# Optimization experiments

Hardware: AMD Instinct MI355X
Metric: run time of the kernel (lower is better)

The kernel has to match this reference:

```python
import jax, jax.numpy as jnp
from jax import lax
import numpy as np

D = 1024      # d_model
H = 16        # n_heads == n_v_heads
DK = 64       # head_k_dim = d_model // n_heads
DV = 128      # head_v_dim = head_dim * expand_v (2.0)
KDIM = H * DK   # 1024
VDIM = H * DV   # 2048
CONV_K = 4
B, T = 2, 4096
EPS = 1e-5


def setup_inputs() -> dict:
    key = jax.random.key(0)
    ks = jax.random.split(key, 14)
    def w(k, shape, s=0.02):
        return jax.random.normal(k, shape, jnp.float32) * s
    return {
        "x": jax.random.normal(ks[0], (B, T, D), jnp.float32),
        "w_q": w(ks[1], (D, KDIM)),
        "w_k": w(ks[2], (D, KDIM)),
        "w_v": w(ks[3], (D, VDIM)),
        "w_a": w(ks[4], (D, H)),
        "w_b": w(ks[5], (D, H)),
        "w_g": w(ks[6], (D, VDIM)),
        "w_out": w(ks[7], (VDIM, D)),
        "A_log": jnp.log(jax.random.uniform(ks[8], (H,), jnp.float32, 1.0, 16.0)),
        "dt_bias": jax.random.uniform(ks[9], (H,), jnp.float32, -4.0, -1.0),
        "conv_q": w(ks[10], (KDIM, CONV_K), 0.1),
        "conv_k": w(ks[11], (KDIM, CONV_K), 0.1),
        "conv_v": w(ks[12], (VDIM, CONV_K), 0.1),
        "norm_w": jnp.ones((DV,), jnp.float32),
    }


def _causal_conv_silu(x, w):
    # x: [B,T,C], w: [C,Kw]  depthwise causal conv1d followed by SiLU
    C = x.shape[-1]
    Kw = w.shape[-1]
    xp = jnp.pad(x, ((0, 0), (Kw - 1, 0), (0, 0))).transpose(0, 2, 1)  # [B,C,T+Kw-1]
    y = lax.conv_general_dilated(
        xp, w[:, None, :], window_strides=(1,), padding="VALID",
        feature_group_count=C, dimension_numbers=("NCH", "OIH", "NCH"))
    return jax.nn.silu(y.transpose(0, 2, 1))  # [B,T,C]


def _l2norm(x, eps=1e-6):
    return x * lax.rsqrt(jnp.sum(x * x, axis=-1, keepdims=True) + eps)


def _gated_delta_rule(q, k, v, g, beta):
    # q,k: [B,T,H,DK] (l2-normalized), v: [B,T,H,DV], g,beta: [B,T,H]
    scale = q.shape[-1] ** -0.5
    qs = jnp.moveaxis(q, 1, 0)
    ks_ = jnp.moveaxis(k, 1, 0)
    vs = jnp.moveaxis(v, 1, 0)
    gs = jnp.moveaxis(g, 1, 0)
    bs = jnp.moveaxis(beta, 1, 0)

    def step(S, inp):
        q_t, k_t, v_t, g_t, b_t = inp
        S = S * jnp.exp(g_t)[..., None, None]            # gated decay
        mem = jnp.einsum("bhk,bhkv->bhv", k_t, S)        # current memory readout
        delta = (v_t - mem) * b_t[..., None]             # beta-weighted delta
        S = S + jnp.einsum("bhk,bhv->bhkv", k_t, delta)  # delta-rule update
        o_t = jnp.einsum("bhk,bhkv->bhv", q_t * scale, S)
        return S, o_t

    S0 = jnp.zeros((q.shape[0], q.shape[2], q.shape[3], v.shape[3]), q.dtype)
    _, o = lax.scan(step, S0, (qs, ks_, vs, gs, bs))
    return jnp.moveaxis(o, 0, 1)  # [B,T,H,DV]


def reference(x, w_q, w_k, w_v, w_a, w_b, w_g, w_out, A_log, dt_bias,
              conv_q, conv_k, conv_v, norm_w):
    Bx, Tx, _ = x.shape
    q = x @ w_q
    k = x @ w_k
    v = x @ w_v
    beta = jax.nn.sigmoid(x @ w_b) * 2.0                      # allow_neg_eigval
    g = -jnp.exp(A_log) * jax.nn.softplus((x @ w_a) + dt_bias)  # [B,T,H]

    q = _causal_conv_silu(q, conv_q)
    k = _causal_conv_silu(k, conv_k)
    v = _causal_conv_silu(v, conv_v)

    q = q.reshape(Bx, Tx, H, DK)
    k = k.reshape(Bx, Tx, H, DK)
    v = v.reshape(Bx, Tx, H, DV)

    # use_qk_l2norm_in_kernel=True
    q = _l2norm(q)
    k = _l2norm(k)

    o = _gated_delta_rule(q, k, v, g, beta)  # [B,T,H,DV]

    # gated RMSNorm: normalize o, gate with silu(w_g(x))
    g_gate = (x @ w_g).reshape(Bx, Tx, H, DV)
    rms = o * lax.rsqrt(jnp.mean(o * o, axis=-1, keepdims=True) + EPS)
    y = rms * norm_w * jax.nn.silu(g_gate)
    return y.reshape(Bx, Tx, VDIM) @ w_out
```

## Files before the change

### kernel.cpp

```cpp
#include <hip/hip_runtime.h>
#include <hip/hip_bf16.h>
#include <math.h>

#define Bc 2
#define Tc 4096
#define Dc 1024
#define Hc 16
#define DKc 64
#define DVc 128
#define KDIMc 1024
#define VDIMc 2048
#define Mrows (Bc*Tc)
#define CC 64
#define NCH (Tc/CC)

typedef short short8 __attribute__((ext_vector_type(8)));
typedef float f32x4 __attribute__((ext_vector_type(4)));

__device__ __forceinline__ float siluf(float x) {
    return x / (1.f + expf(-x));
}
__device__ __forceinline__ float dot4(float4 a, float4 b) {
    return a.x * b.x + a.y * b.y + a.z * b.z + a.w * b.w;
}
__device__ __forceinline__ unsigned short f2bf(float f) {
    unsigned int u = __float_as_uint(f);
    unsigned int r = (u + 0x7fffu + ((u >> 16) & 1u)) >> 16;
    return (unsigned short)r;
}
__device__ __forceinline__ unsigned int pk2(float a, float b) {
    return (unsigned)f2bf(a) | ((unsigned)f2bf(b) << 16);
}
__device__ __forceinline__ float bf2f(unsigned short s) {
    unsigned int u = ((unsigned int)s) << 16;
    return __uint_as_float(u);
}
__device__ __forceinline__ void gload16(const unsigned short* g,
                                        unsigned short* l) {
    __builtin_amdgcn_global_load_lds(
        (const __attribute__((address_space(1))) unsigned int*)g,
        (__attribute__((address_space(3))) unsigned int*)l, 16, 0, 0);
}

__global__ void __launch_bounds__(256) convert_bf16(
    const float* __restrict__ in, unsigned short* __restrict__ out, int n4) {
    int g = blockIdx.x * 256 + threadIdx.x;
    if (g >= n4) return;
    float4 v = *(const float4*)&in[(size_t)g * 4];
    *(uint2*)&out[(size_t)g * 4] = make_uint2(pk2(v.x, v.y), pk2(v.z, v.w));
}

__global__ void __launch_bounds__(256) transp_bf16(
    const float* __restrict__ in, unsigned short* __restrict__ out, int K,
    int N) {
    __shared__ float t[32][33];
    const int nbx = N >> 5;
    const int n0 = (blockIdx.x % nbx) << 5;
    const int k0 = (blockIdx.x / nbx) << 5;
    const int c = threadIdx.x & 31, r4 = (threadIdx.x >> 5) << 2;
#pragma unroll
    for (int i = 0; i < 4; i++)
        t[r4 + i][c] = in[(size_t)(k0 + r4 + i) * N + n0 + c];
    __syncthreads();
#pragma unroll
    for (int i = 0; i < 4; i++)
        out[(size_t)(n0 + r4 + i) * K + k0 + c] = f2bf(t[c][r4 + i]);
}

__global__ void __launch_bounds__(256) transp_f32w(
    const float* __restrict__ in, float* __restrict__ out) {
    __shared__ float t[64][17];
    const int k0 = blockIdx.x * 64;
    const int r = threadIdx.x >> 2, c4 = (threadIdx.x & 3) << 2;
    float4 v = *(const float4*)&in[(size_t)(k0 + r) * 16 + c4];
    t[r][c4 + 0] = v.x;
    t[r][c4 + 1] = v.y;
    t[r][c4 + 2] = v.z;
    t[r][c4 + 3] = v.w;
    __syncthreads();
    const int n = threadIdx.x >> 4;
    const int kk = (threadIdx.x & 15) << 2;
    out[(size_t)n * Dc + k0 + kk + 0] = t[kk + 0][n];
    out[(size_t)n * Dc + k0 + kk + 1] = t[kk + 1][n];
    out[(size_t)n * Dc + k0 + kk + 2] = t[kk + 2][n];
    out[(size_t)n * Dc + k0 + kk + 3] = t[kk + 3][n];
}

__global__ void __launch_bounds__(256) transp_k16(
    const unsigned short* __restrict__ in, unsigned short* __restrict__ out) {
    __shared__ unsigned short t[64][68];
    const int bx = blockIdx.x & 63;
    const int by = (blockIdx.x >> 6) & 15;
    const int b = blockIdx.x >> 10;
    const int t0 = bx << 6, c0 = by << 6;
    {
        const int row = threadIdx.x >> 2, c16 = (threadIdx.x & 3) << 4;
        const unsigned short* src =
            &in[((size_t)b * Tc + t0 + row) * KDIMc + c0 + c16];
#pragma unroll
        for (int i = 0; i < 4; i++)
            *(uint2*)&t[row][c16 + i * 4] = *(const uint2*)&src[i * 4];
    }
    __syncthreads();
    {
        const int cc = threadIdx.x & 63, tp = (threadIdx.x >> 6) << 4;
        unsigned short v[16];
#pragma unroll
        for (int i = 0; i < 16; i++) v[i] = t[tp + i][cc];
        unsigned short* dst =
            &out[((size_t)b * KDIMc + c0 + cc) * Tc + t0 + tp];
        *(uint4*)&dst[0] = *(uint4*)&v[0];
        *(uint4*)&dst[8] = *(uint4*)&v[8];
    }
}

#define GEMM_SHARED()                                                         \
    __shared__ unsigned short As[2][2][128 * 32];                             \
    __shared__ unsigned short Bs[2][2][128 * 32];

#define GEMM_STAGE64(Ap, Bp, Kk, D, KT)                                       \
    {                                                                         \
        const size_t kb0 = (size_t)((KT) << 6) + gcol;                        \
        const size_t kb1 = kb0 + 32;                                          \
        _Pragma("unroll") for (int r = 0; r < 2; r++) {                       \
            const int rows = r * 64 + w * 16;                                 \
            gload16(&Ap[(size_t)(m0 + rows + grow) * Kk + kb0],               \
                    &As[D][0][rows * 32]);                                    \
            gload16(&Ap[(size_t)(m0 + rows + grow) * Kk + kb1],               \
                    &As[D][1][rows * 32]);                                    \
            gload16(&Bp[(size_t)(n0 + rows + grow) * Kk + kb0],               \
                    &Bs[D][0][rows * 32]);                                    \
            gload16(&Bp[(size_t)(n0 + rows + grow) * Kk + kb1],               \
                    &Bs[D][1][rows * 32]);                                    \
        }                                                                     \
    }

#define GEMM_MFMA64(D)                                                        \
    {                                                                         \
        short8 af[4], bfr[4];                                                 \
        _Pragma("unroll") for (int i = 0; i < 4; i++)                         \
            af[i] = *(const short8*)&As[D][0][(wr + i * 16 + fr) * 32 + fk8]; \
        _Pragma("unroll") for (int j = 0; j < 4; j++)                         \
            bfr[j] = *(const short8*)&Bs[D][0][(wc + j * 16 + fr) * 32 + fk8];\
        _Pragma("unroll") for (int i = 0; i < 4; i++)                         \
            _Pragma("unroll") for (int j = 0; j < 4; j++)                     \
                acc[i][j] = __builtin_amdgcn_mfma_f32_16x16x32_bf16(          \
                    af[i], bfr[j], acc[i][j], 0, 0, 0);                       \
        _Pragma("unroll") for (int i = 0; i < 4; i++)                         \
            af[i] = *(const short8*)&As[D][1][(wr + i * 16 + fr) * 32 + fk8]; \
        _Pragma("unroll") for (int j = 0; j < 4; j++)                         \
            bfr[j] = *(const short8*)&Bs[D][1][(wc + j * 16 + fr) * 32 + fk8];\
        _Pragma("unroll") for (int i = 0; i < 4; i++)                         \
            _Pragma("unroll") for (int j = 0; j < 4; j++)                     \
                acc[i][j] = __builtin_amdgcn_mfma_f32_16x16x32_bf16(          \
                    af[i], bfr[j], acc[i][j], 0, 0, 0);                       \
    }

#define GEMM_KLOOP(Ap, Bp, Kk)                                                \
    {                                                                         \
        int cur = 0;                                                          \
        const int nkt = (Kk) >> 6;                                            \
        GEMM_STAGE64(Ap, Bp, Kk, 0, 0);                                       \
        for (int kt = 0; kt < nkt; kt++) {                                    \
            __syncthreads();       \
            if (kt + 1 < nkt) GEMM_STAGE64(Ap, Bp, Kk, cur ^ 1, kt + 1);      \
            GEMM_MFMA64(cur);                                                 \
            cur ^= 1;                                                         \
        }                                                                     \
    }

__global__ void __launch_bounds__(256) gemm_qkv(
    const unsigned short* __restrict__ A, const unsigned short* __restrict__ Bt,
    unsigned short* __restrict__ q16, unsigned short* __restrict__ k16,
    float* __restrict__ vb) {
    GEMM_SHARED();
    const int tid = threadIdx.x;
    const int bx = blockIdx.x & 31, by = blockIdx.x >> 5;
    const int m0 = by << 7, n0 = bx << 7;
    const int w = tid >> 6, lane = tid & 63;
    const int wr = (w >> 1) << 6, wc = (w & 1) << 6;
    const int fr = lane & 15, fk8 = (lane >> 4) << 3;
    const int grow = lane >> 2;
    const int gcol = (lane & 3) << 3;

    f32x4 acc[4][4];
#pragma unroll
    for (int i = 0; i < 4; i++)
#pragma unroll
        for (int j = 0; j < 4; j++)
            acc[i][j] = (f32x4){0.f, 0.f, 0.f, 0.f};

    GEMM_KLOOP(A, Bt, Dc);

    const int cr = (lane >> 4) << 2;
    if (bx < 16) {
        unsigned short* Cb = (bx < 8) ? q16 : k16;
        const int coloff = (bx & 7) << 7;
#pragma unroll
        for (int i = 0; i < 4; i++)
#pragma unroll
            for (int j = 0; j < 4; j++) {
#pragma unroll
                for (int r = 0; r < 4; r++) {
                    Cb[(size_t)(m0 + wr + i * 16 + cr + r) * KDIMc + coloff +
                       wc + j * 16 + fr] = f2bf(acc[i][j][r]);
                }
            }
    } else {
        const int coloff = (bx - 16) << 7;
#pragma unroll
        for (int i = 0; i < 4; i++)
#pragma unroll
            for (int j = 0; j < 4; j++) {
#pragma unroll
                for (int r = 0; r < 4; r++) {
                    vb[(size_t)(m0 + wr + i * 16 + cr + r) * VDIMc + coloff +
                       wc + j * 16 + fr] = acc[i][j][r];
                }
            }
    }
}

__global__ void __launch_bounds__(256) gemm_bf16(
    const unsigned short* __restrict__ A, const unsigned short* __restrict__ Bt,
    float* __restrict__ C, int M, int N, int K) {
    GEMM_SHARED();
    const int tid = threadIdx.x;
    const int nbx = N >> 7;
    const int bx = blockIdx.x % nbx, by = blockIdx.x / nbx;
    const int m0 = by << 7, n0 = bx << 7;
    const int w = tid >> 6, lane = tid & 63;
    const int wr = (w >> 1) << 6, wc = (w & 1) << 6;
    const int fr = lane & 15, fk8 = (lane >> 4) << 3;
    const int grow = lane >> 2;
    const int gcol = (lane & 3) << 3;

    f32x4 acc[4][4];
#pragma unroll
    for (int i = 0; i < 4; i++)
#pragma unroll
        for (int j = 0; j < 4; j++)
            acc[i][j] = (f32x4){0.f, 0.f, 0.f, 0.f};

    GEMM_KLOOP(A, Bt, K);

    const int cr = (lane >> 4) << 2;
#pragma unroll
    for (int i = 0; i < 4; i++)
#pragma unroll
        for (int j = 0; j < 4; j++) {
#pragma unroll
            for (int r = 0; r < 4; r++) {
                C[(size_t)(m0 + wr + i * 16 + cr + r) * N + n0 + wc + j * 16 +
                  fr] = acc[i][j][r];
            }
        }
}

__global__ void __launch_bounds__(256) gemm_gate_rms(
    const unsigned short* __restrict__ A, const unsigned short* __restrict__ Bt,
    const float* __restrict__ o, const float* __restrict__ rfac,
    const float* __restrict__ norm_w, unsigned short* __restrict__ out,
    int M, int N, int K) {
    GEMM_SHARED();
    const int tid = threadIdx.x;
    const int nbx = N >> 7;
    const int bx = blockIdx.x % nbx, by = blockIdx.x / nbx;
    const int m0 = by << 7, n0 = bx << 7;
    const int h = n0 >> 7;
    const int w = tid >> 6, lane = tid & 63;
    const int wr = (w >> 1) << 6, wc = (w & 1) << 6;
    const int fr = lane & 15, fk8 = (lane >> 4) << 3;
    const int grow = lane >> 2;
    const int gcol = (lane & 3) << 3;

    f32x4 acc[4][4];
#pragma unroll
    for (int i = 0; i < 4; i++)
#pragma unroll
        for (int j = 0; j < 4; j++)
            acc[i][j] = (f32x4){0.f, 0.f, 0.f, 0.f};

    GEMM_KLOOP(A, Bt, K);

    const int cr = (lane >> 4) << 2;
#pragma unroll
    for (int i = 0; i < 4; i++)
#pragma unroll
        for (int j = 0; j < 4; j++) {
            const int colh = wc + j * 16 + fr;
            const float nw = norm_w[colh];
#pragma unroll
            for (int r = 0; r < 4; r++) {
                const int row = m0 + wr + i * 16 + cr + r;
                float ov = o[(size_t)row * VDIMc + n0 + colh];
                float f = rfac[(size_t)row * Hc + h];
                float y = ov * f * nw * siluf(acc[i][j][r]);
                out[(size_t)row * VDIMc + n0 + colh] = f2bf(y);
            }
        }
}

__global__ void __launch_bounds__(256) rfac_kernel(
    const float* __restrict__ o, float* __restrict__ rf) {
    const int row = blockIdx.x * 4 + (threadIdx.x >> 6);
    const int lane = threadIdx.x & 63;
    const size_t base = (size_t)row * DVc;
    float2 ov = *(const float2*)&o[base + lane * 2];
    float ss = ov.x * ov.x + ov.y * ov.y;
#pragma unroll
    for (int m = 1; m < 64; m <<= 1) ss += __shfl_xor(ss, m, 64);
    if (lane == 0) rf[row] = rsqrtf(ss * (1.f / 128.f) + 1e-5f);
}

__global__ void __launch_bounds__(256) ab_proj(
    const float* __restrict__ x, const float* __restrict__ w_aT,
    const float* __restrict__ w_bT, const float* __restrict__ A_log,
    const float* __restrict__ dt_bias, float* __restrict__ g_out,
    float* __restrict__ beta_out) {
    const int wv = threadIdx.x >> 6;
    const int lane = threadIdx.x & 63;
    const int h = lane >> 2, kg = lane & 3;
    const int row0 = blockIdx.x * 16 + wv * 4;
    const float* wa = w_aT + (size_t)h * Dc + kg * 256;
    const float* wb = w_bT + (size_t)h * Dc + kg * 256;
    const float* xr = x + (size_t)row0 * Dc + kg * 256;
    float pa[4] = {0.f, 0.f, 0.f, 0.f}, pb[4] = {0.f, 0.f, 0.f, 0.f};
#pragma unroll 4
    for (int k = 0; k < 256; k += 4) {
        float4 a4 = *(const float4*)&wa[k];
        float4 b4 = *(const float4*)&wb[k];
#pragma unroll
        for (int r = 0; r < 4; r++) {
            float4 x4 = *(const float4*)&xr[(size_t)r * Dc + k];
            pa[r] += dot4(x4, a4);
            pb[r] += dot4(x4, b4);
        }
    }
#pragma unroll
    for (int r = 0; r < 4; r++) {
        pa[r] += __shfl_xor(pa[r], 1, 64);
        pa[r] += __shfl_xor(pa[r], 2, 64);
        pb[r] += __shfl_xor(pb[r], 1, 64);
        pb[r] += __shfl_xor(pb[r], 2, 64);
    }
    if (kg == 0) {
        const float el = expf(A_log[h]);
        const float db = dt_bias[h];
#pragma unroll
        for (int r = 0; r < 4; r++) {
            float arg = pa[r] + db;
            float sp = fmaxf(arg, 0.f) + log1pf(expf(-fabsf(arg)));
            g_out[(size_t)(row0 + r) * Hc + h] = -el * sp;
            beta_out[(size_t)(row0 + r) * Hc + h] =
                2.f / (1.f + expf(-pb[r]));
        }
    }
}

template <int C>
__global__ void __launch_bounds__(256) save_halo(
    const float* __restrict__ in, float* __restrict__ halo) {
    const int g = blockIdx.x * 256 + threadIdx.x;
    const int total = Bc * (Tc / 64 - 1) * 3 * C;
    if (g >= total) return;
    const int c = g % C;
    int r = g / C;
    const int j = r % 3;
    r /= 3;
    const int chunk = r % (Tc / 64 - 1) + 1;
    const int b = r / (Tc / 64 - 1);
    halo[((size_t)(b * 64 + chunk) * 3 + j) * C + c] =
        in[((size_t)b * Tc + chunk * 64 - 3 + j) * C + c];
}

template <int C, bool L2N>
__global__ void __launch_bounds__(256) conv_silu_b2b(
    const unsigned short* __restrict__ in, const float* __restrict__ w,
    unsigned short* __restrict__ out) {
    constexpr int CB = C / 256;
    const int bidx = blockIdx.x;
    const int cb = bidx % CB;
    const int tchunk = (bidx / CB) % (Tc / 64);
    const int b = bidx / (CB * (Tc / 64));
    const int c = cb * 256 + threadIdx.x;
    const int t0 = tchunk * 64;
    const float w0 = w[c * 4 + 0], w1 = w[c * 4 + 1], w2 = w[c * 4 + 2],
                w3 = w[c * 4 + 3];
    const unsigned short* src = in + (size_t)b * Tc * C + c;
    float xm3 = (t0 >= 3) ? bf2f(src[(size_t)(t0 - 3) * C]) : 0.f;
    float xm2 = (t0 >= 2) ? bf2f(src[(size_t)(t0 - 2) * C]) : 0.f;
    float xm1 = (t0 >= 1) ? bf2f(src[(size_t)(t0 - 1) * C]) : 0.f;
    unsigned short* dst = out + (size_t)b * Tc * C + c;
#pragma unroll 4
    for (int i = 0; i < 64; i++) {
        float xt = bf2f(src[(size_t)(t0 + i) * C]);
        float y = w0 * xm3 + w1 * xm2 + w2 * xm1 + w3 * xt;
        y = siluf(y);
        if (L2N) {
            float ss = y * y;
#pragma unroll
            for (int m = 1; m < 64; m <<= 1) ss += __shfl_xor(ss, m, 64);
            y *= rsqrtf(ss + 1e-6f);
        }
        dst[(size_t)(t0 + i) * C] = f2bf(y);
        xm3 = xm2;
        xm2 = xm1;
        xm1 = xt;
    }
}

template <int C, bool L2N>
__global__ void __launch_bounds__(256) conv_silu_inplace(
    float* __restrict__ buf, const float* __restrict__ w,
    const float* __restrict__ halo) {
    constexpr int CB = C / 256;
    const int bidx = blockIdx.x;
    const int cb = bidx % CB;
    const int tchunk = (bidx / CB) % (Tc / 64);
    const int b = bidx / (CB * (Tc / 64));
    const int c = cb * 256 + threadIdx.x;
    const int t0 = tchunk * 64;
    const float w0 = w[c * 4 + 0], w1 = w[c * 4 + 1], w2 = w[c * 4 + 2],
                w3 = w[c * 4 + 3];
    float xm3 = 0.f, xm2 = 0.f, xm1 = 0.f;
    if (tchunk > 0) {
        const float* hp = halo + (size_t)(b * 64 + tchunk) * 3 * C + c;
        xm3 = hp[0];
        xm2 = hp[C];
        xm1 = hp[2 * C];
    }
    float* p = buf + (size_t)b * Tc * C + c;
#pragma unroll 4
    for (int i = 0; i < 64; i++) {
        float xt = p[(size_t)(t0 + i) * C];
        float y = w0 * xm3 + w1 * xm2 + w2 * xm1 + w3 * xt;
        y = siluf(y);
        if (L2N) {
            float ss = y * y;
#pragma unroll
            for (int m = 1; m < 64; m <<= 1) ss += __shfl_xor(ss, m, 64);
            y *= rsqrtf(ss + 1e-6f);
        }
        p[(size_t)(t0 + i) * C] = y;
        xm3 = xm2;
        xm2 = xm1;
        xm1 = xt;
    }
}

__global__ void __launch_bounds__(256) tm_precompute(
    const unsigned short* __restrict__ kc, const unsigned short* __restrict__ qc,
    const float* __restrict__ g, const float* __restrict__ beta,
    unsigned short* __restrict__ tmT, unsigned short* __restrict__ tmM) {
    const int bid = blockIdx.x;
    const int ch = bid & (NCH - 1);
    const int bh = bid >> 6;
    const int b = bh >> 4, h = bh & 15;
    const int tid = threadIdx.x;
    const int t0 = ch * CC;

    __shared__ __align__(16) unsigned short kb16[CC][72];
    __shared__ __align__(16) unsigned short qb16[CC][72];
    __shared__ __align__(16) float AtL[CC][DKc + 4];
    __shared__ float cL[CC], betaL[CC];

    const size_t qk0 = (size_t)b * Tc * KDIMc + h * DKc;
    const size_t gb0 = (size_t)b * Tc * Hc + h;
    const size_t tile = (size_t)(bh * NCH + ch) * 4096;

#pragma unroll
    for (int i = 0; i < 2; i++) {
        int e = tid + i * 256;
        int r = e >> 3, c8 = (e & 7) << 3;
        *(short8*)&kb16[r][c8] =
            *(const short8*)&kc[qk0 + (size_t)(t0 + r) * KDIMc + c8];
        *(short8*)&qb16[r][c8] =
            *(const short8*)&qc[qk0 + (size_t)(t0 + r) * KDIMc + c8];
    }
    if (tid < 64) {
        float gv = g[gb0 + (size_t)(t0 + tid) * Hc];
        float cv = gv;
#pragma unroll
        for (int d = 1; d < 64; d <<= 1) {
            float nb = __shfl_up(cv, d, 64);
            if (tid >= d) cv += nb;
        }
        cL[tid] = cv;
        betaL[tid] = beta[gb0 + (size_t)(t0 + tid) * Hc];
    }
    __syncthreads();

    {
        const int w = tid >> 6, lane = tid & 63;
        const int fr = lane & 15, fk8 = (lane >> 4) << 3;
        const int rr = (lane >> 4) << 2;
        short8 ak0 = *(const short8*)&kb16[w * 16 + fr][fk8];
        short8 ak1 = *(const short8*)&kb16[w * 16 + fr][fk8 + 32];
        short8 aq0 = *(const short8*)&qb16[w * 16 + fr][fk8];
        short8 aq1 = *(const short8*)&qb16[w * 16 + fr][fk8 + 32];
#pragma unroll
        for (int j = 0; j < 4; j++) {
            short8 b0 = *(const short8*)&kb16[j * 16 + fr][fk8];
            short8 b1 = *(const short8*)&kb16[j * 16 + fr][fk8 + 32];
            f32x4 kk = (f32x4){0.f, 0.f, 0.f, 0.f};
            f32x4 qk = (f32x4){0.f, 0.f, 0.f, 0.f};
            kk = __builtin_amdgcn_mfma_f32_16x16x32_bf16(ak0, b0, kk, 0, 0, 0);
            kk = __builtin_amdgcn_mfma_f32_16x16x32_bf16(ak1, b1, kk, 0, 0, 0);
            qk = __builtin_amdgcn_mfma_f32_16x16x32_bf16(aq0, b0, qk, 0, 0, 0);
            qk = __builtin_amdgcn_mfma_f32_16x16x32_bf16(aq1, b1, qk, 0, 0, 0);
#pragma unroll
            for (int r = 0; r < 4; r++) {
                int t = w * 16 + rr + r, s = j * 16 + fr;
                float E = expf(cL[t] - cL[s]);
                AtL[s][t] = (s < t) ? betaL[t] * E * kk[r] : 0.f;
                tmM[tile + (size_t)t * 64 + s] =
                    (s <= t) ? f2bf(0.125f * E * qk[r]) : (unsigned short)0;
            }
        }
    }
    __syncthreads();

    {
        const int w = tid >> 6, lane = tid & 63;
        float acc[16];
#pragma unroll
        for (int di = 0; di < 16; di++)
            acc[di] = (lane == w * 16 + di) ? 1.f : 0.f;
#pragma unroll 4
        for (int s = 0; s < 64; s++) {
            float a = AtL[s][lane];
#pragma unroll
            for (int di = 0; di < 16; di++) {
                float ds = __shfl(acc[di], s, 64);
                acc[di] -= a * ds;
            }
        }
        unsigned short tb[16];
#pragma unroll
        for (int di = 0; di < 16; di++) tb[di] = f2bf(acc[di]);
        *(uint4*)&tmT[tile + (size_t)lane * 64 + w * 16] = *(uint4*)&tb[0];
        *(uint4*)&tmT[tile + (size_t)lane * 64 + w * 16 + 8] = *(uint4*)&tb[8];
    }
}

__global__ void __launch_bounds__(512, 2) delta_scan(
    const unsigned short* __restrict__ kc, const unsigned short* __restrict__ qc,
    const unsigned short* __restrict__ kcT,
    float* vo, const float* __restrict__ g, const float* __restrict__ beta,
    const unsigned short* __restrict__ tmT,
    const unsigned short* __restrict__ tmM) {
    const int bid = blockIdx.x;
    const int sl = bid >> 5;
    const int bh = bid & 31;
    const int b = bh >> 4, h = bh & 15;
    const int tid = threadIdx.x;

    __shared__ __align__(16) float VL[CC][20];
    __shared__ float gamL[CC], egL[CC], betaL[CC];
    __shared__ __align__(16) unsigned short kb16[CC][72];
    __shared__ __align__(16) unsigned short kh16[CC][72];
    __shared__ __align__(16) unsigned short qb16[CC][72];
    __shared__ __align__(16) unsigned short Tb16[CC][72];
    __shared__ __align__(16) unsigned short Mb16[CC][72];
    __shared__ __align__(16) unsigned short STb16[16][72];
    __shared__ __align__(16) unsigned short DTb16[16][72];
    __shared__ __align__(16) unsigned short D2b16[16][72];
    __shared__ __align__(16) unsigned short egd16[16][72];

    const size_t qk0 = (size_t)b * Tc * KDIMc + h * DKc;
    const size_t kT0 = ((size_t)b * KDIMc + h * DKc) * Tc;
    const size_t v0 = (size_t)b * Tc * VDIMc + h * DVc + sl * 16;
    const size_t gb0 = (size_t)b * Tc * Hc + h;
    const size_t tb0 = (size_t)(bh * NCH) * 4096;

    for (int i = tid; i < 16 * 72; i += 512) ((unsigned short*)STb16)[i] = 0;

    const int r8 = tid >> 3, c8 = (tid & 7) << 3;
    const int wid = tid >> 6, lane = tid & 63;
    const int fr = lane & 15;
    const int fk8 = (lane >> 4) << 3;
    const int rr = (lane >> 4) << 2;

    f32x4 accS = (f32x4){0.f, 0.f, 0.f, 0.f};

    short8 kv, kvT, qv, tv, mv;
    float4 vv0;
    float gvr = 0.f, bvr = 0.f;

#define LOADREGS(CH)                                                          \
    {                                                                         \
        const size_t tK = qk0 + (size_t)(CH) * CC * KDIMc;                    \
        const size_t tile_ = tb0 + (size_t)(CH) * 4096;                       \
        kv = *(const short8*)&kc[tK + (size_t)r8 * KDIMc + c8];               \
        kvT = *(const short8*)&kcT[kT0 + (size_t)r8 * Tc + (CH) * CC + c8];   \
        qv = *(const short8*)&qc[tK + (size_t)r8 * KDIMc + c8];               \
        tv = *(const short8*)&tmT[tile_ + (size_t)tid * 8];                   \
        mv = *(const short8*)&tmM[tile_ + (size_t)tid * 8];                   \
        if (tid < 256)                                                        \
            vv0 = *(const float4*)&vo[v0 +                                    \
                                      (size_t)((CH) * CC + (tid >> 2)) *     \
                                          VDIMc +                             \
                                      ((tid & 3) << 2)];                      \
        if (tid < 64) {                                                       \
            gvr = g[gb0 + (size_t)((CH) * CC + tid) * Hc];                    \
            bvr = beta[gb0 + (size_t)((CH) * CC + tid) * Hc];                 \
        }                                                                     \
    }

    LOADREGS(0);

#pragma unroll 1
    for (int ch = 0; ch < NCH; ch++) {
        __syncthreads();

        {
            *(short8*)&kb16[r8][c8] = kv;
            *(short8*)&kh16[r8][c8] = kvT;
            *(short8*)&qb16[r8][c8] = qv;
            *(short8*)&Tb16[r8][c8] = tv;
            *(short8*)&Mb16[r8][c8] = mv;
            if (tid < 256) *(float4*)&VL[tid >> 2][(tid & 3) << 2] = vv0;
            if (tid < 64) {
                float cv = gvr;
#pragma unroll
                for (int d = 1; d < 64; d <<= 1) {
                    float nb = __shfl_up(cv, d, 64);
                    if (tid >= d) cv += nb;
                }
                gamL[tid] = expf(cv);
                float cend = __shfl(cv, 63, 64);
                egL[tid] = expf(cend - cv);
                betaL[tid] = bvr;
            }
        }
        if (ch + 1 < NCH) LOADREGS(ch + 1);
        __syncthreads();

        f32x4 acc1 = (f32x4){0.f, 0.f, 0.f, 0.f};
        {
            short8 bs0 = *(const short8*)&STb16[fr][fk8];
            short8 bs1 = *(const short8*)&STb16[fr][fk8 + 32];
            if (wid < 4) {
                const int m0 = wid << 4;
                short8 a0 = *(const short8*)&kb16[m0 + fr][fk8];
                short8 a1 = *(const short8*)&kb16[m0 + fr][fk8 + 32];
                acc1 = __builtin_amdgcn_mfma_f32_16x16x32_bf16(a0, bs0, acc1, 0, 0, 0);
                acc1 = __builtin_amdgcn_mfma_f32_16x16x32_bf16(a1, bs1, acc1, 0, 0, 0);
#pragma unroll
                for (int r = 0; r < 4; r++) {
                    int t = m0 + rr + r;
                    float rhs = betaL[t] * (VL[t][fr] - gamL[t] * acc1[r]);
                    DTb16[fr][t] = f2bf(rhs);
                }
            } else {
                const int m0 = (wid - 4) << 4;
                short8 a0 = *(const short8*)&qb16[m0 + fr][fk8];
                short8 a1 = *(const short8*)&qb16[m0 + fr][fk8 + 32];
                acc1 = __builtin_amdgcn_mfma_f32_16x16x32_bf16(a0, bs0, acc1, 0, 0, 0);
                acc1 = __builtin_amdgcn_mfma_f32_16x16x32_bf16(a1, bs1, acc1, 0, 0, 0);
#pragma unroll
                for (int r = 0; r < 4; r++) {
                    int t = m0 + rr + r;
                    acc1[r] *= 0.125f * gamL[t];
                }
            }
        }
        __syncthreads();

        if (wid < 4) {
            const int m0 = wid << 4;
            short8 a0 = *(const short8*)&Tb16[m0 + fr][fk8];
            short8 a1 = *(const short8*)&Tb16[m0 + fr][fk8 + 32];
            short8 b0 = *(const short8*)&DTb16[fr][fk8];
            short8 b1 = *(const short8*)&DTb16[fr][fk8 + 32];
            f32x4 d = (f32x4){0.f, 0.f, 0.f, 0.f};
            d = __builtin_amdgcn_mfma_f32_16x16x32_bf16(a0, b0, d, 0, 0, 0);
            d = __builtin_amdgcn_mfma_f32_16x16x32_bf16(a1, b1, d, 0, 0, 0);
#pragma unroll
            for (int r = 0; r < 4; r++) {
                int t = m0 + rr + r;
                D2b16[fr][t] = f2bf(d[r]);
                egd16[fr][t] = f2bf(egL[t] * d[r]);
            }
        }
        __syncthreads();

        if (wid >= 4) {
            const int m0 = (wid - 4) << 4;
            short8 a0 = *(const short8*)&Mb16[m0 + fr][fk8];
            short8 a1 = *(const short8*)&Mb16[m0 + fr][fk8 + 32];
            short8 b0 = *(const short8*)&D2b16[fr][fk8];
            short8 b1 = *(const short8*)&D2b16[fr][fk8 + 32];
            f32x4 o = acc1;
            o = __builtin_amdgcn_mfma_f32_16x16x32_bf16(a0, b0, o, 0, 0, 0);
            o = __builtin_amdgcn_mfma_f32_16x16x32_bf16(a1, b1, o, 0, 0, 0);
#pragma unroll
            for (int r = 0; r < 4; r++)
                vo[v0 + (size_t)(ch * CC + m0 + rr + r) * VDIMc + fr] = o[r];
        } else {
            const int m0 = wid << 4;
            const float ge = gamL[63];
            short8 a0 = *(const short8*)&kh16[m0 + fr][fk8];
            short8 a1 = *(const short8*)&kh16[m0 + fr][fk8 + 32];
            short8 b0 = *(const short8*)&egd16[fr][fk8];
            short8 b1 = *(const short8*)&egd16[fr][fk8 + 32];
#pragma unroll
            for (int r = 0; r < 4; r++) accS[r] *= ge;
            accS = __builtin_amdgcn_mfma_f32_16x16x32_bf16(a0, b0, accS, 0, 0, 0);
            accS = __builtin_amdgcn_mfma_f32_16x16x32_bf16(a1, b1, accS, 0, 0, 0);
#pragma unroll
            for (int r = 0; r < 4; r++)
                STb16[fr][m0 + rr + r] = f2bf(accS[r]);
        }
    }
#undef LOADREGS
}

extern "C" void kernel_launch(void* const* d_in, const int* in_sizes, int n_in,
                              void* d_out, int out_size, void* d_ws,
                              size_t ws_size, hipStream_t stream) {
    const float* x = (const float*)d_in[0];
    const float* w_q = (const float*)d_in[1];
    const float* w_k = (const float*)d_in[2];
    const float* w_v = (const float*)d_in[3];
    const float* w_a = (const float*)d_in[4];
    const float* w_b = (const float*)d_in[5];
    const float* w_g = (const float*)d_in[6];
    const float* w_out = (const float*)d_in[7];
    const float* A_log = (const float*)d_in[8];
    const float* dt_bias = (const float*)d_in[9];
    const float* conv_q = (const float*)d_in[10];
    const float* conv_k = (const float*)d_in[11];
    const float* conv_v = (const float*)d_in[12];
    const float* norm_w = (const float*)d_in[13];

    float* ws = (float*)d_ws;
    const size_t M = Mrows;
    float* qb = ws;
    float* kb = qb + M * KDIMc;
    float* vb = kb + M * KDIMc;
    float* tm = vb + M * VDIMc;
    float* gbuf = tm + M * VDIMc;
    float* bbuf = gbuf + M * Hc;
    float* xtra = bbuf + M * Hc;

    unsigned short* q16raw = (unsigned short*)qb;
    unsigned short* k16raw = (unsigned short*)kb;
    unsigned short* kcT16 = (unsigned short*)qb;
    unsigned short* tmS = (unsigned short*)tm;
    unsigned short* tmT16 = tmS;
    unsigned short* tmM16 = tmS + (size_t)8388608;
    unsigned short* qc16 = tmS + (size_t)16777216;
    unsigned short* kc16 = tmS + (size_t)25165824;
    float* halo = tm;
    unsigned short* obb = tmS;
    float* rfac = gbuf;

    unsigned short* xb = (unsigned short*)xtra;
    unsigned short* wqT = xb + M * KDIMc;
    unsigned short* wkT = wqT + (size_t)KDIMc * Dc;
    unsigned short* wvT = wkT + (size_t)KDIMc * Dc;
    unsigned short* wgT = wvT + (size_t)VDIMc * Dc;
    unsigned short* woT = wgT + (size_t)VDIMc * Dc;
    float* waT = (float*)(woT + (size_t)Dc * VDIMc);
    float* wbT = waT + (size_t)16 * Dc;

    convert_bf16<<<dim3(M * Dc / 4 / 256), 256, 0, stream>>>(x, xb, M * Dc / 4);
    transp_bf16<<<dim3((KDIMc / 32) * (Dc / 32)), 256, 0, stream>>>(w_q, wqT,
                                                                    Dc, KDIMc);
    transp_bf16<<<dim3((KDIMc / 32) * (Dc / 32)), 256, 0, stream>>>(w_k, wkT,
                                                                    Dc, KDIMc);
    transp_bf16<<<dim3((VDIMc / 32) * (Dc / 32)), 256, 0, stream>>>(w_v, wvT,
                                                                    Dc, VDIMc);
    transp_bf16<<<dim3((VDIMc / 32) * (Dc / 32)), 256, 0, stream>>>(w_g, wgT,
                                                                    Dc, VDIMc);
    transp_bf16<<<dim3((Dc / 32) * (VDIMc / 32)), 256, 0, stream>>>(
        w_out, woT, VDIMc, Dc);
    transp_f32w<<<dim3(Dc / 64), 256, 0, stream>>>(w_a, waT);
    transp_f32w<<<dim3(Dc / 64), 256, 0, stream>>>(w_b, wbT);

    gemm_qkv<<<dim3((M / 128) * 32), 256, 0, stream>>>(xb, wqT, q16raw, k16raw,
                                                       vb);

    ab_proj<<<dim3(M / 16), 256, 0, stream>>>(x, waT, wbT, A_log, dt_bias,
                                              gbuf, bbuf);

    conv_silu_b2b<KDIMc, true>
        <<<dim3(Bc * (Tc / 64) * (KDIMc / 256)), 256, 0, stream>>>(
            q16raw, conv_q, qc16);
    conv_silu_b2b<KDIMc, true>
        <<<dim3(Bc * (Tc / 64) * (KDIMc / 256)), 256, 0, stream>>>(
            k16raw, conv_k, kc16);
    transp_k16<<<dim3(Bc * 16 * 64), 256, 0, stream>>>(kc16, kcT16);
    {
        const int nv = Bc * (Tc / 64 - 1) * 3 * VDIMc;
        save_halo<VDIMc><<<dim3((nv + 255) / 256), 256, 0, stream>>>(vb, halo);
        conv_silu_inplace<VDIMc, false>
            <<<dim3(Bc * (Tc / 64) * (VDIMc / 256)), 256, 0, stream>>>(
                vb, conv_v, halo);
    }

    tm_precompute<<<dim3(Bc * Hc * NCH), 256, 0, stream>>>(
        kc16, qc16, gbuf, bbuf, tmT16, tmM16);
    delta_scan<<<dim3(Bc * Hc * 8), 512, 0, stream>>>(
        kc16, qc16, kcT16, vb, gbuf, bbuf, tmT16, tmM16);

    rfac_kernel<<<dim3(M * Hc / 4), 256, 0, stream>>>(vb, rfac);
    gemm_gate_rms<<<dim3((M / 128) * (VDIMc / 128)), 256, 0, stream>>>(
        xb, wgT, vb, rfac, norm_w, obb, M, VDIMc, Dc);

    gemm_bf16<<<dim3((M / 128) * (Dc / 128)), 256, 0, stream>>>(
        obb, woT, (float*)d_out, M, Dc, VDIMc);
}
```

Before: 604.1 us.

## Store scan output as bf16 and single-buffer the GEMM k-loop

The delta-scan output is now written in bf16 to a separate buffer, and the RMS-factor and gated-norm kernels read bf16 instead of fp32, which halves that traffic. Separately, the shared GEMM k-loop drops its double-buffered LDS prefetch in favour of a single buffer with two barriers per iteration. That cuts LDS use and may raise occupancy, but global loads no longer overlap the MFMA work, which risks slowing every GEMM. The bf16 output also loses some precision before normalization.

```diff
diff --git a/kernel.cpp b/kernel.cpp
--- a/kernel.cpp
+++ b/kernel.cpp
@@ -115,41 +115,41 @@
 }
 
 #define GEMM_SHARED()                                                         \
-    __shared__ unsigned short As[2][2][128 * 32];                             \
-    __shared__ unsigned short Bs[2][2][128 * 32];
-
-#define GEMM_STAGE64(Ap, Bp, Kk, D, KT)                                       \
+    __shared__ unsigned short As0[128 * 32], As1[128 * 32];                   \
+    __shared__ unsigned short Bs0[128 * 32], Bs1[128 * 32];
+
+#define GEMM_STAGE64(Ap, Bp, Kk)                                              \
     {                                                                         \
-        const size_t kb0 = (size_t)((KT) << 6) + gcol;                        \
+        const size_t kb0 = (size_t)(kt << 6) + gcol;                          \
         const size_t kb1 = kb0 + 32;                                          \
         _Pragma("unroll") for (int r = 0; r < 2; r++) {                       \
             const int rows = r * 64 + w * 16;                                 \
             gload16(&Ap[(size_t)(m0 + rows + grow) * Kk + kb0],               \
-                    &As[D][0][rows * 32]);                                    \
+                    &As0[rows * 32]);                                         \
             gload16(&Ap[(size_t)(m0 + rows + grow) * Kk + kb1],               \
-                    &As[D][1][rows * 32]);                                    \
+                    &As1[rows * 32]);                                         \
             gload16(&Bp[(size_t)(n0 + rows + grow) * Kk + kb0],               \
-                    &Bs[D][0][rows * 32]);                                    \
+                    &Bs0[rows * 32]);                                         \
             gload16(&Bp[(size_t)(n0 + rows + grow) * Kk + kb1],               \
-                    &Bs[D][1][rows * 32]);                                    \
+                    &Bs1[rows * 32]);                                         \
         }                                                                     \
     }
 
-#define GEMM_MFMA64(D)                                                        \
+#define GEMM_MFMA64()                                                         \
     {                                                                         \
         short8 af[4], bfr[4];                                                 \
         _Pragma("unroll") for (int i = 0; i < 4; i++)                         \
-            af[i] = *(const short8*)&As[D][0][(wr + i * 16 + fr) * 32 + fk8]; \
+            af[i] = *(const short8*)&As0[(wr + i * 16 + fr) * 32 + fk8];      \
         _Pragma("unroll") for (int j = 0; j < 4; j++)                         \
-            bfr[j] = *(const short8*)&Bs[D][0][(wc + j * 16 + fr) * 32 + fk8];\
+            bfr[j] = *(const short8*)&Bs0[(wc + j * 16 + fr) * 32 + fk8];     \
         _Pragma("unroll") for (int i = 0; i < 4; i++)                         \
             _Pragma("unroll") for (int j = 0; j < 4; j++)                     \
                 acc[i][j] = __builtin_amdgcn_mfma_f32_16x16x32_bf16(          \
                     af[i], bfr[j], acc[i][j], 0, 0, 0);                       \
         _Pragma("unroll") for (int i = 0; i < 4; i++)                         \
-            af[i] = *(const short8*)&As[D][1][(wr + i * 16 + fr) * 32 + fk8]; \
+            af[i] = *(const short8*)&As1[(wr + i * 16 + fr) * 32 + fk8];      \
         _Pragma("unroll") for (int j = 0; j < 4; j++)                         \
-            bfr[j] = *(const short8*)&Bs[D][1][(wc + j * 16 + fr) * 32 + fk8];\
+            bfr[j] = *(const short8*)&Bs1[(wc + j * 16 + fr) * 32 + fk8];     \
         _Pragma("unroll") for (int i = 0; i < 4; i++)                         \
             _Pragma("unroll") for (int j = 0; j < 4; j++)                     \
                 acc[i][j] = __builtin_amdgcn_mfma_f32_16x16x32_bf16(          \
@@ -158,14 +158,12 @@
 
 #define GEMM_KLOOP(Ap, Bp, Kk)                                                \
     {                                                                         \
-        int cur = 0;                                                          \
         const int nkt = (Kk) >> 6;                                            \
-        GEMM_STAGE64(Ap, Bp, Kk, 0, 0);                                       \
         for (int kt = 0; kt < nkt; kt++) {                                    \
-            __syncthreads();       \
-            if (kt + 1 < nkt) GEMM_STAGE64(Ap, Bp, Kk, cur ^ 1, kt + 1);      \
-            GEMM_MFMA64(cur);                                                 \
-            cur ^= 1;                                                         \
+            __syncthreads();                                                  \
+            GEMM_STAGE64(Ap, Bp, Kk);                                         \
+            __syncthreads();                                                  \
+            GEMM_MFMA64();                                                    \
         }                                                                     \
     }
 
@@ -259,7 +257,7 @@
 
 __global__ void __launch_bounds__(256) gemm_gate_rms(
     const unsigned short* __restrict__ A, const unsigned short* __restrict__ Bt,
-    const float* __restrict__ o, const float* __restrict__ rfac,
+    const unsigned short* __restrict__ o, const float* __restrict__ rfac,
     const float* __restrict__ norm_w, unsigned short* __restrict__ out,
     int M, int N, int K) {
     GEMM_SHARED();
@@ -293,7 +291,7 @@
 #pragma unroll
             for (int r = 0; r < 4; r++) {
                 const int row = m0 + wr + i * 16 + cr + r;
-                float ov = o[(size_t)row * VDIMc + n0 + colh];
+                float ov = bf2f(o[(size_t)row * VDIMc + n0 + colh]);
                 float f = rfac[(size_t)row * Hc + h];
                 float y = ov * f * nw * siluf(acc[i][j][r]);
                 out[(size_t)row * VDIMc + n0 + colh] = f2bf(y);
@@ -302,12 +300,14 @@
 }
 
 __global__ void __launch_bounds__(256) rfac_kernel(
-    const float* __restrict__ o, float* __restrict__ rf) {
+    const unsigned short* __restrict__ o, float* __restrict__ rf) {
     const int row = blockIdx.x * 4 + (threadIdx.x >> 6);
     const int lane = threadIdx.x & 63;
     const size_t base = (size_t)row * DVc;
-    float2 ov = *(const float2*)&o[base + lane * 2];
-    float ss = ov.x * ov.x + ov.y * ov.y;
+    unsigned int pv = *(const unsigned int*)&o[base + lane * 2];
+    float o0 = bf2f((unsigned short)(pv & 0xffff));
+    float o1 = bf2f((unsigned short)(pv >> 16));
+    float ss = o0 * o0 + o1 * o1;
 #pragma unroll
     for (int m = 1; m < 64; m <<= 1) ss += __shfl_xor(ss, m, 64);
     if (lane == 0) rf[row] = rsqrtf(ss * (1.f / 128.f) + 1e-5f);
@@ -547,7 +547,8 @@
 __global__ void __launch_bounds__(512, 2) delta_scan(
     const unsigned short* __restrict__ kc, const unsigned short* __restrict__ qc,
     const unsigned short* __restrict__ kcT,
-    float* vo, const float* __restrict__ g, const float* __restrict__ beta,
+    const float* __restrict__ vc, unsigned short* __restrict__ o16,
+    const float* __restrict__ g, const float* __restrict__ beta,
     const unsigned short* __restrict__ tmT,
     const unsigned short* __restrict__ tmM) {
     const int bid = blockIdx.x;
@@ -598,7 +599,7 @@
         tv = *(const short8*)&tmT[tile_ + (size_t)tid * 8];                   \
         mv = *(const short8*)&tmM[tile_ + (size_t)tid * 8];                   \
         if (tid < 256)                                                        \
-            vv0 = *(const float4*)&vo[v0 +                                    \
+            vv0 = *(const float4*)&vc[v0 +                                    \
                                       (size_t)((CH) * CC + (tid >> 2)) *     \
                                           VDIMc +                             \
                                       ((tid & 3) << 2)];                      \
@@ -697,7 +698,8 @@
             o = __builtin_amdgcn_mfma_f32_16x16x32_bf16(a1, b1, o, 0, 0, 0);
 #pragma unroll
             for (int r = 0; r < 4; r++)
-                vo[v0 + (size_t)(ch * CC + m0 + rr + r) * VDIMc + fr] = o[r];
+                o16[v0 + (size_t)(ch * CC + m0 + rr + r) * VDIMc + fr] =
+                    f2bf(o[r]);
         } else {
             const int m0 = wid << 4;
             const float ge = gamL[63];
@@ -748,6 +750,7 @@
     unsigned short* q16raw = (unsigned short*)qb;
     unsigned short* k16raw = (unsigned short*)kb;
     unsigned short* kcT16 = (unsigned short*)qb;
+    unsigned short* o16 = (unsigned short*)kb;
     unsigned short* tmS = (unsigned short*)tm;
     unsigned short* tmT16 = tmS;
     unsigned short* tmM16 = tmS + (size_t)8388608;
@@ -804,11 +807,11 @@
     tm_precompute<<<dim3(Bc * Hc * NCH), 256, 0, stream>>>(
         kc16, qc16, gbuf, bbuf, tmT16, tmM16);
     delta_scan<<<dim3(Bc * Hc * 8), 512, 0, stream>>>(
-        kc16, qc16, kcT16, vb, gbuf, bbuf, tmT16, tmM16);
-
-    rfac_kernel<<<dim3(M * Hc / 4), 256, 0, stream>>>(vb, rfac);
+        kc16, qc16, kcT16, vb, o16, gbuf, bbuf, tmT16, tmM16);
+
+    rfac_kernel<<<dim3(M * Hc / 4), 256, 0, stream>>>(o16, rfac);
     gemm_gate_rms<<<dim3((M / 128) * (VDIMc / 128)), 256, 0, stream>>>(
-        xb, wgT, vb, rfac, norm_w, obb, M, VDIMc, Dc);
+        xb, wgT, o16, rfac, norm_w, obb, M, VDIMc, Dc);
 
     gemm_bf16<<<dim3((M / 128) * (Dc / 128)), 256, 0, stream>>>(
         obb, woT, (float*)d_out, M, Dc, VDIMc);
```

After: 604.6 us. Within noise of the previous version (+0.1%).
